# Optimization experiments

Measured on AMD Instinct MI355X. Metric: run time of the kernel, lower is better.

The kernel has to match this reference:

```python
import jax, jax.numpy as jnp
import numpy as np
from jax.scipy.special import logsumexp

N = 4096          # nodes per graph
E = 65536         # edges per graph
HID = 128
HEADS = 4
HD = HID // HEADS
L_GNN = 2
L_CROSS = 3
SINK_ITERS = 20
LN_EPS = 1e-5
SCALE = 1.0 / np.sqrt(HD)


def layer_norm(x, g, b):
    m = jnp.mean(x, axis=-1, keepdims=True)
    v = jnp.mean((x - m) ** 2, axis=-1, keepdims=True)
    return (x - m) * jax.lax.rsqrt(v + LN_EPS) * g + b


def gcn_conv(x, ei, w, b):
    # PyG GCNConv: self-loops + symmetric normalization, sum aggregation
    n = x.shape[0]
    xl = x @ w                                  # [n, hid]
    loops = jnp.arange(n, dtype=ei.dtype)
    src = jnp.concatenate([ei[0], loops])
    dst = jnp.concatenate([ei[1], loops])
    deg = jax.ops.segment_sum(jnp.ones_like(src, dtype=x.dtype), dst, num_segments=n)
    dinv = jnp.where(deg > 0, jax.lax.rsqrt(deg), 0.0)
    norm = dinv[src] * dinv[dst]                # [E+n]
    msg = xl[src] * norm[:, None]
    return jax.ops.segment_sum(msg, dst, num_segments=n) + b


def encode(x, ei, gcn_w, gcn_b, ln_g, ln_b):
    h = x
    for l in range(L_GNN):
        h = gcn_conv(h, ei, gcn_w[l], gcn_b[l])
        h = layer_norm(h, ln_g[l], ln_b[l])
        h = jax.nn.relu(h)
    return h


def attend(X, Y, wq, wk, wv, wo, bo):
    # X attends to Y; residual add
    n, m = X.shape[0], Y.shape[0]
    Q = (X @ wq).reshape(n, HEADS, HD).transpose(1, 0, 2)   # [h, n, d]
    K = (Y @ wk).reshape(m, HEADS, HD).transpose(1, 0, 2)
    V = (Y @ wv).reshape(m, HEADS, HD).transpose(1, 0, 2)
    scores = jnp.einsum('hnd,hmd->hnm', Q, K) * SCALE
    attn = jax.nn.softmax(scores, axis=-1)
    O = jnp.einsum('hnm,hmd->hnd', attn, V)                 # [h, n, d]
    O = O.transpose(1, 0, 2).reshape(n, HID)
    return O @ wo + bo + X


def sinkhorn(log_alpha, n_iters=SINK_ITERS):
    def body(i, lp):
        lp = lp - logsumexp(lp, axis=1, keepdims=True)  # row normalize
        lp = lp - logsumexp(lp, axis=0, keepdims=True)  # col normalize
        return lp
    log_p = jax.lax.fori_loop(0, n_iters, body, log_alpha)
    return jnp.exp(log_p)


def setup_inputs() -> dict:
    key = jax.random.key(0)
    ks = jax.random.split(key, 24)
    f32 = jnp.float32
    w = lambda k, *s: jax.random.normal(k, s, dtype=f32) * 0.05
    inp = {
        'A_x': jax.random.normal(ks[0], (N, HID), dtype=f32),
        'A_ei': jax.random.randint(ks[1], (2, E), 0, N),
        'B_x': jax.random.normal(ks[2], (N, HID), dtype=f32),
        'B_ei': jax.random.randint(ks[3], (2, E), 0, N),
        'in_proj_w': w(ks[4], HID, HID),
        'in_proj_b': jnp.zeros((HID,), f32),
        'gcn_w': w(ks[5], L_GNN, HID, HID),
        'gcn_b': jnp.zeros((L_GNN, HID), f32),
        'gcn_ln_g': jnp.ones((L_GNN, HID), f32),
        'gcn_ln_b': jnp.zeros((L_GNN, HID), f32),
        'cross_q': w(ks[6], L_CROSS, HID, HID),
        'cross_k': w(ks[7], L_CROSS, HID, HID),
        'cross_v': w(ks[8], L_CROSS, HID, HID),
        'cross_o': w(ks[9], L_CROSS, HID, HID),
        'cross_o_b': jnp.zeros((L_CROSS, HID), f32),
        'post_ln_g': jnp.ones((HID,), f32),
        'post_ln_b': jnp.zeros((HID,), f32),
        'proj_w': w(ks[10], HID, HID),
        'proj_b': jnp.zeros((HID,), f32),
        'null_vec': jax.random.normal(ks[11], (HID,), dtype=f32) * 0.01,
        'cp_w1': w(ks[12], HID, HID),
        'cp_b1': jnp.zeros((HID,), f32),
        'cp_w2': w(ks[13], HID, HID),
        'cp_b2': jnp.zeros((HID,), f32),
    }
    return inp


def reference(A_x, A_ei, B_x, B_ei, in_proj_w, in_proj_b, gcn_w, gcn_b,
              gcn_ln_g, gcn_ln_b, cross_q, cross_k, cross_v, cross_o,
              cross_o_b, post_ln_g, post_ln_b, proj_w, proj_b, null_vec,
              cp_w1, cp_b1, cp_w2, cp_b2):
    A_in = A_x @ in_proj_w + in_proj_b
    B_in = B_x @ in_proj_w + in_proj_b
    A_h = encode(A_in, A_ei, gcn_w, gcn_b, gcn_ln_g, gcn_ln_b)
    B_h = encode(B_in, B_ei, gcn_w, gcn_b, gcn_ln_g, gcn_ln_b)
    for l in range(L_CROSS):
        A_new = attend(A_h, B_h, cross_q[l], cross_k[l], cross_v[l], cross_o[l], cross_o_b[l])
        B_new = attend(B_h, A_h, cross_q[l], cross_k[l], cross_v[l], cross_o[l], cross_o_b[l])
        A_h, B_h = A_new, B_new
    A_h = layer_norm(A_h, post_ln_g, post_ln_b)
    B_h = layer_norm(B_h, post_ln_g, post_ln_b)
    A_p = A_h @ proj_w + proj_b
    B_p = B_h @ proj_w + proj_b
    inv_sqrt_d = 1.0 / np.sqrt(HID)
    logits = (A_p @ B_p.T) * inv_sqrt_d                    # [N, N]
    null_col = (A_p @ null_vec) * inv_sqrt_d               # [N]
    logits_with_null = jnp.concatenate([logits, null_col[:, None]], axis=1)
    P = sinkhorn(logits_with_null)
    zA = jax.nn.relu(A_p @ cp_w1 + cp_b1) @ cp_w2 + cp_b2
    zB = jax.nn.relu(B_p @ cp_w1 + cp_b1) @ cp_w2 + cp_b2
    return (logits_with_null, P, zA, zB)
```

## Files before the change

kernel.cpp:

```cpp
#include <hip/hip_runtime.h>
#include <hip/hip_bf16.h>
#include <math.h>

#define NN 4096
#define EE 65536
#define HID_ 128
#define HDIM 32
#define NCOL 4097
#define EHP 4104

static constexpr float SCALE_ATT = 0.17677669529663687f;
static constexpr float INV_SQRT_D = 0.08838834764831845f;
static constexpr float LOG2E = 1.4426950408889634f;

typedef __attribute__((ext_vector_type(8))) short bf16x8;
typedef __attribute__((ext_vector_type(4))) float f32x4;
typedef _Float16 half8 __attribute__((ext_vector_type(8)));
typedef _Float16 half4v __attribute__((ext_vector_type(4)));

__device__ __forceinline__ float wred64(float v) {
#pragma unroll
  for (int m = 32; m > 0; m >>= 1) v += __shfl_xor(v, m, 64);
  return v;
}

__device__ __forceinline__ ushort f2b(float f) {
  __hip_bfloat16 h = __float2bfloat16(f);
  union { __hip_bfloat16 h; ushort u; } c;
  c.h = h;
  return c.u;
}

__device__ __forceinline__ unsigned pack2bf(float e0, float e1) {
  return ((__float_as_uint(e1) + 0x8000u) & 0xffff0000u) |
         ((__float_as_uint(e0) + 0x8000u) >> 16);
}

template <bool BIAS, bool RELU, bool RESID, bool BCAST>
__global__ __launch_bounds__(256, 2) void gemm128_k(
    const float* __restrict__ x0, const float* __restrict__ x1,
    const float* __restrict__ w, const float* __restrict__ bias,
    const float* __restrict__ res0, const float* __restrict__ res1,
    float* __restrict__ o0, float* __restrict__ o1,
    ushort* __restrict__ ob0, ushort* __restrict__ ob1) {
  const float* x = blockIdx.y ? x1 : x0;
  const float* res = blockIdx.y ? res1 : res0;
  float* out = blockIdx.y ? o1 : o0;
  ushort* outb = blockIdx.y ? ob1 : ob0;
  __shared__ float Xs[32][132];
  __shared__ float Ws[32][128];
  const int tid = threadIdx.x;
  const int rowbase = blockIdx.x * 32;
#pragma unroll
  for (int i = 0; i < 4; ++i) {
    int lin = tid + i * 256;
    int r = lin >> 5, c4 = lin & 31;
    *(float4*)&Xs[r][c4 * 4] =
        *(const float4*)&x[(size_t)(rowbase + r) * HID_ + c4 * 4];
  }
  float acc[4][4] = {};
  const int tr = tid >> 5, tc = tid & 31;
  const int r0 = tr * 4, c0 = tc * 4;
  for (int k0 = 0; k0 < 128; k0 += 32) {
    __syncthreads();
#pragma unroll
    for (int i = 0; i < 4; ++i) {
      int lin = tid + i * 256;
      int r = lin >> 5, c4 = lin & 31;
      *(float4*)&Ws[r][c4 * 4] =
          *(const float4*)&w[(size_t)(k0 + r) * HID_ + c4 * 4];
    }
    __syncthreads();
#pragma unroll
    for (int kk = 0; kk < 32; kk += 4) {
      float4 wv0 = *(const float4*)&Ws[kk + 0][c0];
      float4 wv1 = *(const float4*)&Ws[kk + 1][c0];
      float4 wv2 = *(const float4*)&Ws[kk + 2][c0];
      float4 wv3 = *(const float4*)&Ws[kk + 3][c0];
#pragma unroll
      for (int r = 0; r < 4; ++r) {
        float4 xv = *(const float4*)&Xs[r0 + r][k0 + kk];
        acc[r][0] += xv.x * wv0.x + xv.y * wv1.x + xv.z * wv2.x + xv.w * wv3.x;
        acc[r][1] += xv.x * wv0.y + xv.y * wv1.y + xv.z * wv2.y + xv.w * wv3.y;
        acc[r][2] += xv.x * wv0.z + xv.y * wv1.z + xv.z * wv2.z + xv.w * wv3.z;
        acc[r][3] += xv.x * wv0.w + xv.y * wv1.w + xv.z * wv2.w + xv.w * wv3.w;
      }
    }
  }
  float4 bv = make_float4(0.f, 0.f, 0.f, 0.f);
  if (BIAS) bv = *(const float4*)&bias[c0];
#pragma unroll
  for (int r = 0; r < 4; ++r) {
    size_t orow = (size_t)(rowbase + r0 + r) * HID_ + c0;
    float4 ov;
    ov.x = acc[r][0] + bv.x;
    ov.y = acc[r][1] + bv.y;
    ov.z = acc[r][2] + bv.z;
    ov.w = acc[r][3] + bv.w;
    if (RESID) {
      float4 rv = *(const float4*)&res[orow];
      ov.x += rv.x; ov.y += rv.y; ov.z += rv.z; ov.w += rv.w;
    }
    if (RELU) {
      ov.x = fmaxf(ov.x, 0.f); ov.y = fmaxf(ov.y, 0.f);
      ov.z = fmaxf(ov.z, 0.f); ov.w = fmaxf(ov.w, 0.f);
    }
    *(float4*)&out[orow] = ov;
    if (BCAST) {
      *(ushort4*)&outb[orow] =
          make_ushort4(f2b(ov.x), f2b(ov.y), f2b(ov.z), f2b(ov.w));
    }
  }
}

__global__ __launch_bounds__(256, 2) void gemm_qkv_k(
    const float* __restrict__ x0, const float* __restrict__ x1,
    const float* __restrict__ wq, const float* __restrict__ wk,
    const float* __restrict__ wv, ushort* __restrict__ QA,
    ushort* __restrict__ QB, ushort* __restrict__ KA, ushort* __restrict__ KB,
    ushort* __restrict__ VA, ushort* __restrict__ VB) {
  const int z = blockIdx.z;
  const float* x = blockIdx.y ? x1 : x0;
  const float* w = (z == 0) ? wq : (z == 1 ? wk : wv);
  ushort* out = (z == 0) ? (blockIdx.y ? QB : QA)
                         : (z == 1 ? (blockIdx.y ? KB : KA)
                                   : (blockIdx.y ? VB : VA));
  const float scale = (z == 0) ? SCALE_ATT * LOG2E : 1.f;
  __shared__ float Xs[32][132];
  __shared__ float Ws[32][128];
  const int tid = threadIdx.x;
  const int rowbase = blockIdx.x * 32;
#pragma unroll
  for (int i = 0; i < 4; ++i) {
    int lin = tid + i * 256;
    int r = lin >> 5, c4 = lin & 31;
    *(float4*)&Xs[r][c4 * 4] =
        *(const float4*)&x[(size_t)(rowbase + r) * HID_ + c4 * 4];
  }
  float acc[4][4] = {};
  const int tr = tid >> 5, tc = tid & 31;
  const int r0 = tr * 4, c0 = tc * 4;
  for (int k0 = 0; k0 < 128; k0 += 32) {
    __syncthreads();
#pragma unroll
    for (int i = 0; i < 4; ++i) {
      int lin = tid + i * 256;
      int r = lin >> 5, c4 = lin & 31;
      *(float4*)&Ws[r][c4 * 4] =
          *(const float4*)&w[(size_t)(k0 + r) * HID_ + c4 * 4];
    }
    __syncthreads();
#pragma unroll
    for (int kk = 0; kk < 32; kk += 4) {
      float4 wv0 = *(const float4*)&Ws[kk + 0][c0];
      float4 wv1 = *(const float4*)&Ws[kk + 1][c0];
      float4 wv2 = *(const float4*)&Ws[kk + 2][c0];
      float4 wv3 = *(const float4*)&Ws[kk + 3][c0];
#pragma unroll
      for (int r = 0; r < 4; ++r) {
        float4 xv = *(const float4*)&Xs[r0 + r][k0 + kk];
        acc[r][0] += xv.x * wv0.x + xv.y * wv1.x + xv.z * wv2.x + xv.w * wv3.x;
        acc[r][1] += xv.x * wv0.y + xv.y * wv1.y + xv.z * wv2.y + xv.w * wv3.y;
        acc[r][2] += xv.x * wv0.z + xv.y * wv1.z + xv.z * wv2.z + xv.w * wv3.z;
        acc[r][3] += xv.x * wv0.w + xv.y * wv1.w + xv.z * wv2.w + xv.w * wv3.w;
      }
    }
  }
  if (z < 2) {
#pragma unroll
    for (int r = 0; r < 4; ++r) {
      ushort4 pk = make_ushort4(
          f2b(acc[r][0] * scale), f2b(acc[r][1] * scale),
          f2b(acc[r][2] * scale), f2b(acc[r][3] * scale));
      *(ushort4*)&out[(size_t)(rowbase + r0 + r) * HID_ + c0] = pk;
    }
  } else {
#pragma unroll
    for (int r = 0; r < 4; ++r)
#pragma unroll
      for (int c = 0; c < 4; ++c)
        out[(size_t)(c0 + c) * NN + rowbase + r0 + r] = f2b(acc[r][c]);
  }
}

__global__ void count_deg_k(const int* __restrict__ eiA,
                            const int* __restrict__ eiB, int* cntA, int* cntB) {
  int e = blockIdx.x * 256 + threadIdx.x;
  const int* ei = blockIdx.y ? eiB : eiA;
  int* cnt = blockIdx.y ? cntB : cntA;
  atomicAdd(&cnt[ei[EE + e]], 1);
}

__global__ __launch_bounds__(1024) void scan_k(const int* cntA, const int* cntB,
                                               int* rpA, int* rpB, float* dinvA,
                                               float* dinvB) {
  const int* cnt = blockIdx.y ? cntB : cntA;
  int* rp = blockIdx.y ? rpB : rpA;
  float* dinv = blockIdx.y ? dinvB : dinvA;
  __shared__ int part[1024];
  int tid = threadIdx.x;
  int v0 = cnt[tid * 4], v1 = cnt[tid * 4 + 1], v2 = cnt[tid * 4 + 2],
      v3 = cnt[tid * 4 + 3];
  int tot = v0 + v1 + v2 + v3;
  part[tid] = tot;
  __syncthreads();
  int x = tot;
  for (int off = 1; off < 1024; off <<= 1) {
    int y = (tid >= off) ? part[tid - off] : 0;
    __syncthreads();
    x += y;
    part[tid] = x;
    __syncthreads();
  }
  int excl = x - tot;
  rp[tid * 4] = excl;
  rp[tid * 4 + 1] = excl + v0;
  rp[tid * 4 + 2] = excl + v0 + v1;
  rp[tid * 4 + 3] = excl + v0 + v1 + v2;
  if (tid == 1023) rp[4096] = x;
  dinv[tid * 4] = rsqrtf((float)(v0 + 1));
  dinv[tid * 4 + 1] = rsqrtf((float)(v1 + 1));
  dinv[tid * 4 + 2] = rsqrtf((float)(v2 + 1));
  dinv[tid * 4 + 3] = rsqrtf((float)(v3 + 1));
}

__global__ void fill_k(const int* __restrict__ eiA, const int* __restrict__ eiB,
                       const int* rpA, const int* rpB, int* fillA, int* fillB,
                       int* srcA, int* srcB) {
  int e = blockIdx.x * 256 + threadIdx.x;
  const int* ei = blockIdx.y ? eiB : eiA;
  const int* rp = blockIdx.y ? rpB : rpA;
  int* fill = blockIdx.y ? fillB : fillA;
  int* src = blockIdx.y ? srcB : srcA;
  int d = ei[EE + e], s = ei[e];
  int pos = atomicAdd(&fill[d], 1);
  src[rp[d] + pos] = s;
}

__global__ __launch_bounds__(256) void gcn_agg_k(
    const float* __restrict__ xlA, const float* __restrict__ xlB,
    const int* __restrict__ rpA, const int* __restrict__ rpB,
    const int* __restrict__ srcA, const int* __restrict__ srcB,
    const float* __restrict__ dinvA, const float* __restrict__ dinvB,
    const float* __restrict__ gb, const float* __restrict__ lg,
    const float* __restrict__ lb, float* __restrict__ outA,
    float* __restrict__ outB) {
  const float* xl = blockIdx.y ? xlB : xlA;
  const int* rp = blockIdx.y ? rpB : rpA;
  const int* src = blockIdx.y ? srcB : srcA;
  const float* dinv = blockIdx.y ? dinvB : dinvA;
  float* out = blockIdx.y ? outB : outA;
  int wid = threadIdx.x >> 6, lane = threadIdx.x & 63;
  int node = blockIdx.x * 4 + wid;
  int b = rp[node], e = rp[node + 1];
  float di = dinv[node];
  float a0 = 0.f, a1 = 0.f;
  for (int base = b; base < e; base += 64) {
    int rem = e - base;
    int sv = 0;
    float wv = 0.f;
    if (lane < rem) {
      int s = src[base + lane];
      sv = s;
      wv = dinv[s] * di;
    }
    int nch = rem < 64 ? rem : 64;
    for (int j = 0; j < nch; ++j) {
      int s = __shfl(sv, j, 64);
      float w = __shfl(wv, j, 64);
      a0 += xl[(size_t)s * HID_ + lane] * w;
      a1 += xl[(size_t)s * HID_ + 64 + lane] * w;
    }
  }
  a0 += xl[(size_t)node * HID_ + lane] * di * di;
  a1 += xl[(size_t)node * HID_ + 64 + lane] * di * di;
  a0 += gb[lane];
  a1 += gb[64 + lane];
  float mean = wred64(a0 + a1) * (1.f / 128.f);
  float d0 = a0 - mean, d1 = a1 - mean;
  float var = wred64(d0 * d0 + d1 * d1) * (1.f / 128.f);
  float rs = rsqrtf(var + 1e-5f);
  float o0 = d0 * rs * lg[lane] + lb[lane];
  float o1 = d1 * rs * lg[64 + lane] + lb[64 + lane];
  out[(size_t)node * HID_ + lane] = fmaxf(o0, 0.f);
  out[(size_t)node * HID_ + 64 + lane] = fmaxf(o1, 0.f);
}

__global__ __launch_bounds__(256) void ln_k(float* __restrict__ hA,
                                            float* __restrict__ hB,
                                            const float* __restrict__ g,
                                            const float* __restrict__ b) {
  float* h = blockIdx.y ? hB : hA;
  int wid = threadIdx.x >> 6, lane = threadIdx.x & 63;
  int row = blockIdx.x * 4 + wid;
  float a0 = h[(size_t)row * HID_ + lane];
  float a1 = h[(size_t)row * HID_ + 64 + lane];
  float mean = wred64(a0 + a1) * (1.f / 128.f);
  float d0 = a0 - mean, d1 = a1 - mean;
  float var = wred64(d0 * d0 + d1 * d1) * (1.f / 128.f);
  float rs = rsqrtf(var + 1e-5f);
  h[(size_t)row * HID_ + lane] = d0 * rs * g[lane] + b[lane];
  h[(size_t)row * HID_ + 64 + lane] = d1 * rs * g[64 + lane] + b[64 + lane];
}

__global__ __launch_bounds__(256, 4) void attn_mfma_k(
    const ushort* __restrict__ QA, const ushort* __restrict__ KA,
    const ushort* __restrict__ VtA, const ushort* __restrict__ QB,
    const ushort* __restrict__ KB, const ushort* __restrict__ VtB,
    float* __restrict__ Opart, float* __restrict__ lpart) {
  const int qt = blockIdx.x, h = blockIdx.y;
  const int dir = blockIdx.z >> 1, sl = blockIdx.z & 1;
  const ushort* Q = dir ? QB : QA;
  const ushort* K = dir ? KA : KB;
  const ushort* Vt = dir ? VtA : VtB;

  __shared__ ushort KF[2048];
  __shared__ ushort VF[2048];
  __shared__ ushort PF[4][1024];

  const int tid = threadIdx.x;
  const int w = tid >> 6, l = tid & 63;
  const int lr = l & 15, lg = l >> 4;

  const int qrow = qt * 64 + w * 16 + lr;
  bf16x8 qf = *(const bf16x8*)&Q[(size_t)qrow * HID_ + h * HDIM + lg * 8];

  f32x4 oacc0 = {0.f, 0.f, 0.f, 0.f};
  f32x4 oacc1 = {0.f, 0.f, 0.f, 0.f};
  float lsum = 0.f;

  const int ldst = ((w * 4 + lg) * 16 + lr) * 8;
  const ushort* Kg =
      K + (size_t)(sl * 2048 + w * 16 + lr) * HID_ + h * HDIM + lg * 8;
  const ushort* Vg = Vt + (size_t)(h * HDIM + (w >> 1) * 16 + lr) * NN +
                     sl * 2048 + (w & 1) * 32 + lg * 8;

  bf16x8 kreg = *(const bf16x8*)Kg;
  bf16x8 vreg = *(const bf16x8*)Vg;

  for (int t = 0; t < 32; ++t) {
    __syncthreads();
    *(bf16x8*)&KF[ldst] = kreg;
    *(bf16x8*)&VF[ldst] = vreg;
    if (t < 31) {
      kreg = *(const bf16x8*)&Kg[(size_t)(t + 1) * 64 * HID_];
      vreg = *(const bf16x8*)&Vg[(t + 1) * 64];
    }
    __syncthreads();
#pragma unroll
    for (int s = 0; s < 4; ++s) {
      bf16x8 kf = *(const bf16x8*)&KF[((s * 4 + lg) * 16 + lr) * 8];
      f32x4 c = {0.f, 0.f, 0.f, 0.f};
      c = __builtin_amdgcn_mfma_f32_16x16x32_bf16(kf, qf, c, 0, 0, 0);
      float e0 = exp2f(c[0]), e1 = exp2f(c[1]);
      float e2 = exp2f(c[2]), e3 = exp2f(c[3]);
      lsum += (e0 + e1) + (e2 + e3);
      const int k0 = s >> 1;
      const int lgr = (s & 1) * 2 + (lg >> 1);
      const int e8 = (lg & 1) * 4;
      *(uint2*)&PF[w][((k0 * 4 + lgr) * 16 + lr) * 8 + e8] =
          make_uint2(pack2bf(e0, e1), pack2bf(e2, e3));
    }
#pragma unroll
    for (int k0 = 0; k0 < 2; ++k0) {
      bf16x8 pa = *(const bf16x8*)&PF[w][((k0 * 4 + lg) * 16 + lr) * 8];
      bf16x8 vb0 = *(const bf16x8*)&VF[((k0 * 4 + lg) * 16 + lr) * 8];
      bf16x8 vb1 = *(const bf16x8*)&VF[(((2 + k0) * 4 + lg) * 16 + lr) * 8];
      oacc0 = __builtin_amdgcn_mfma_f32_16x16x32_bf16(pa, vb0, oacc0, 0, 0, 0);
      oacc1 = __builtin_amdgcn_mfma_f32_16x16x32_bf16(pa, vb1, oacc1, 0, 0, 0);
    }
  }
  lsum += __shfl_xor(lsum, 16, 64);
  lsum += __shfl_xor(lsum, 32, 64);
  const int pb = sl * 2 + dir;
  if (lg == 0)
    lpart[(size_t)(pb * 4 + h) * NN + qt * 64 + w * 16 + lr] = lsum;
#pragma unroll
  for (int r = 0; r < 4; ++r) {
    int q = qt * 64 + w * 16 + lg * 4 + r;
    Opart[((size_t)pb * NN + q) * HID_ + h * HDIM + lr] = oacc0[r];
    Opart[((size_t)pb * NN + q) * HID_ + h * HDIM + 16 + lr] = oacc1[r];
  }
}

__global__ void attn_combine_k(const float* __restrict__ Opart,
                               const float* __restrict__ lpart,
                               float* __restrict__ outA,
                               float* __restrict__ outB) {
  int row = blockIdx.x, dir = blockIdx.y, f = threadIdx.x;
  int h = f >> 5;
  float o = 0.f, lsum = 0.f;
#pragma unroll
  for (int sl = 0; sl < 2; ++sl) {
    int pb = sl * 2 + dir;
    o += Opart[((size_t)pb * NN + row) * HID_ + f];
    lsum += lpart[(size_t)(pb * 4 + h) * NN + row];
  }
  float* out = dir ? outB : outA;
  out[(size_t)row * HID_ + f] = o / lsum;
}

__global__ __launch_bounds__(256, 2) void gemm_nt_mfma_k(
    const ushort* __restrict__ Apb, const ushort* __restrict__ Bpb,
    float* __restrict__ L, _Float16* __restrict__ Eh) {
  __shared__ ushort As[128 * 128];
  __shared__ ushort Bs[128 * 128];
  const int tid = threadIdx.x;
  const int ab = blockIdx.y * 128, bb = blockIdx.x * 128;
#pragma unroll
  for (int i = 0; i < 8; ++i) {
    int lin = tid + i * 256;
    int row = lin >> 4, ch = lin & 15;
    int pch = ch ^ (row & 15);
    *(bf16x8*)&As[row * 128 + pch * 8] =
        *(const bf16x8*)&Apb[(size_t)(ab + row) * HID_ + ch * 8];
    *(bf16x8*)&Bs[row * 128 + pch * 8] =
        *(const bf16x8*)&Bpb[(size_t)(bb + row) * HID_ + ch * 8];
  }
  __syncthreads();
  const int w = tid >> 6, l = tid & 63, lr = l & 15, lg = l >> 4;
  f32x4 acc[2][8];
#pragma unroll
  for (int fm = 0; fm < 2; ++fm)
#pragma unroll
    for (int nf = 0; nf < 8; ++nf) acc[fm][nf] = {0.f, 0.f, 0.f, 0.f};
#pragma unroll
  for (int kc = 0; kc < 4; ++kc) {
    bf16x8 a0 = *(const bf16x8*)
        &As[((w * 2 + 0) * 16 + lr) * 128 + ((kc * 4 + lg) ^ lr) * 8];
    bf16x8 a1 = *(const bf16x8*)
        &As[((w * 2 + 1) * 16 + lr) * 128 + ((kc * 4 + lg) ^ lr) * 8];
#pragma unroll
    for (int nf = 0; nf < 8; ++nf) {
      bf16x8 bf = *(const bf16x8*)
          &Bs[(nf * 16 + lr) * 128 + ((kc * 4 + lg) ^ lr) * 8];
      acc[0][nf] = __builtin_amdgcn_mfma_f32_16x16x32_bf16(a0, bf, acc[0][nf], 0, 0, 0);
      acc[1][nf] = __builtin_amdgcn_mfma_f32_16x16x32_bf16(a1, bf, acc[1][nf], 0, 0, 0);
    }
  }
#pragma unroll
  for (int fm = 0; fm < 2; ++fm)
#pragma unroll
    for (int nf = 0; nf < 8; ++nf)
#pragma unroll
      for (int r = 0; r < 4; ++r) {
        int row = ab + (w * 2 + fm) * 16 + lg * 4 + r;
        int col = bb + nf * 16 + lr;
        float v = acc[fm][nf][r] * INV_SQRT_D;
        L[(size_t)row * NCOL + col] = v;
        Eh[(size_t)row * EHP + col] = (_Float16)exp2f(v * LOG2E);
      }
}

__global__ void null_col_k(const float* __restrict__ Ap,
                           const float* __restrict__ nv, float* __restrict__ L,
                           _Float16* __restrict__ Eh) {
  int row = blockIdx.x, lane = threadIdx.x;
  float s = Ap[(size_t)row * HID_ + lane] * nv[lane] +
            Ap[(size_t)row * HID_ + 64 + lane] * nv[64 + lane];
  s = wred64(s);
  if (lane == 0) {
    float v = s * INV_SQRT_D;
    L[(size_t)row * NCOL + 4096] = v;
    Eh[(size_t)row * EHP + 4096] = (_Float16)exp2f(v * LOG2E);
  }
  if (lane >= 1 && lane < 8) Eh[(size_t)row * EHP + 4096 + lane] = (_Float16)0.f;
}

__global__ __launch_bounds__(256) void sink_fused_k(
    const _Float16* __restrict__ Eh, const float* __restrict__ t_old,
    float* __restrict__ t_new, float* __restrict__ colpart,
    float* __restrict__ u) {
  __shared__ float vinv[EHP];
  __shared__ float uls[8];
  const int tid = threadIdx.x, bid = blockIdx.x;
  if (tid < 9) {
    int z = bid * 9 + tid;
    if (z < EHP) t_new[z] = 0.f;
  }
  for (int i = tid; i < EHP; i += 256)
    vinv[i] = (i < NCOL) ? (1.f / t_old[i]) : 0.f;
  __syncthreads();
  const int w = tid >> 6, l = tid & 63;
  const int row0 = bid * 8;
#pragma unroll
  for (int rr = 0; rr < 2; ++rr) {
    int row = row0 + w * 2 + rr;
    const _Float16* Ep = Eh + (size_t)row * EHP;
    float s = 0.f;
    for (int j = l * 4; j < EHP; j += 256) {
      half4v e = *(const half4v*)&Ep[j];
      float4 vv = *(const float4*)&vinv[j];
      s += (float)e[0] * vv.x + (float)e[1] * vv.y + (float)e[2] * vv.z +
           (float)e[3] * vv.w;
    }
    s = wred64(s);
    if (l == 0) {
      float uv = 1.f / s;
      uls[w * 2 + rr] = uv;
      u[row] = uv;
    }
  }
  __syncthreads();
  float ur[8];
#pragma unroll
  for (int r = 0; r < 8; ++r) ur[r] = uls[r];
  float* cp = colpart + (size_t)bid * EHP;
  for (int j = tid * 4; j < EHP; j += 1024) {
    float a0 = 0.f, a1 = 0.f, a2 = 0.f, a3 = 0.f;
#pragma unroll
    for (int r = 0; r < 8; ++r) {
      half4v e = *(const half4v*)&Eh[(size_t)(row0 + r) * EHP + j];
      a0 += (float)e[0] * ur[r];
      a1 += (float)e[1] * ur[r];
      a2 += (float)e[2] * ur[r];
      a3 += (float)e[3] * ur[r];
    }
    *(float4*)&cp[j] = make_float4(a0, a1, a2, a3);
  }
}

__global__ __launch_bounds__(256) void sink_reduce_k(
    const float* __restrict__ colpart, float* __restrict__ t_new) {
  int j = blockIdx.x * 256 + threadIdx.x;
  if (j >= EHP) return;
  int b0 = blockIdx.y * 64;
  float s = 0.f;
#pragma unroll 8
  for (int b = 0; b < 64; ++b) s += colpart[(size_t)(b0 + b) * EHP + j];
  atomicAdd(&t_new[j], s);
}

__global__ void sink_init_k(float* t0) {
  int j = blockIdx.x * 256 + threadIdx.x;
  if (j < EHP) t0[j] = 1.f;
}

__global__ __launch_bounds__(256) void sink_finalE_k(
    const _Float16* __restrict__ Eh, const float* __restrict__ u,
    const float* __restrict__ t, float* __restrict__ P) {
  __shared__ float vls[NCOL];
  int tid = threadIdx.x, row = blockIdx.x;
  for (int i = tid; i < NCOL; i += 256) vls[i] = 1.f / t[i];
  __syncthreads();
  float ur = u[row];
  const _Float16* Ep = Eh + (size_t)row * EHP;
  float* Pp = P + (size_t)row * NCOL;
  for (int j = tid; j < NCOL; j += 256) Pp[j] = (float)Ep[j] * ur * vls[j];
}

extern "C" void kernel_launch(void* const* d_in, const int* in_sizes, int n_in,
                              void* d_out, int out_size, void* d_ws,
                              size_t ws_size, hipStream_t stream) {
  const float* A_x = (const float*)d_in[0];
  const int* A_ei = (const int*)d_in[1];
  const float* B_x = (const float*)d_in[2];
  const int* B_ei = (const int*)d_in[3];
  const float* in_w = (const float*)d_in[4];
  const float* in_b = (const float*)d_in[5];
  const float* gcn_w = (const float*)d_in[6];
  const float* gcn_b = (const float*)d_in[7];
  const float* lng = (const float*)d_in[8];
  const float* lnb = (const float*)d_in[9];
  const float* cq = (const float*)d_in[10];
  const float* ck = (const float*)d_in[11];
  const float* cv = (const float*)d_in[12];
  const float* co = (const float*)d_in[13];
  const float* cob = (const float*)d_in[14];
  const float* plg = (const float*)d_in[15];
  const float* plb = (const float*)d_in[16];
  const float* pw = (const float*)d_in[17];
  const float* pb = (const float*)d_in[18];
  const float* nullv = (const float*)d_in[19];
  const float* w1 = (const float*)d_in[20];
  const float* b1 = (const float*)d_in[21];
  const float* w2 = (const float*)d_in[22];
  const float* b2 = (const float*)d_in[23];

  float* ws = (float*)d_ws;
  size_t off = 0;
  auto alloc = [&](size_t n) { float* p = ws + off; off += n; return p; };
  const size_t NHE = (size_t)NN * HID_;
  float* tA = alloc(NHE);
  float* tB = alloc(NHE);
  float* Ap = alloc(NHE);
  float* Bp = alloc(NHE);
  ushort* Apb = (ushort*)alloc(NHE / 2);
  ushort* Bpb = (ushort*)alloc(NHE / 2);
  float* uvec = alloc(NN);
  float* t0 = alloc(EHP);
  float* t1 = alloc(EHP);
  float* zone = ws + off;
  float* hA0 = alloc(NHE); float* hB0 = alloc(NHE);
  float* hA1 = alloc(NHE); float* hB1 = alloc(NHE);
  float* QA = alloc(NHE);  float* KAb = alloc(NHE); float* VAb = alloc(NHE);
  float* QB = alloc(NHE);  float* KBb = alloc(NHE); float* VBb = alloc(NHE);
  float* Opart = alloc(4 * NHE);
  float* lpart = alloc((size_t)16 * NN);
  float* dinvA = alloc(NN); float* dinvB = alloc(NN);
  int* ib = (int*)(ws + off);
  int* cntA = ib;             int* cntB = cntA + NN;
  int* fillA = cntB + NN;     int* fillB = fillA + NN;
  int* rpA = fillB + NN;      int* rpB = rpA + (NN + 1);
  int* srcA = rpB + (NN + 1); int* srcB = srcA + EE;
  size_t ints_floats = (size_t)(4 * NN + 2 * (NN + 1) + 2 * EE);
  _Float16* Eh = (_Float16*)zone;
  {
    size_t named = (size_t)((ws + off) - zone) + ints_floats;
    size_t eh_floats = ((size_t)NN * EHP + 1) / 2;
    size_t need = eh_floats > named ? eh_floats : named;
    off = (size_t)(zone - ws) + need;
  }
  float* colpart = alloc((size_t)512 * EHP);

  float* Lout = (float*)d_out;
  float* Pout = Lout + (size_t)NN * NCOL;
  float* zA = Pout + (size_t)NN * NCOL;
  float* zB = zA + NHE;

  hipMemsetAsync(cntA, 0, 4 * NN * sizeof(int), stream);

  gemm128_k<true, false, false, false><<<dim3(128, 2), 256, 0, stream>>>(
      A_x, B_x, in_w, in_b, nullptr, nullptr, hA0, hB0, nullptr, nullptr);
  count_deg_k<<<dim3(256, 2), 256, 0, stream>>>(A_ei, B_ei, cntA, cntB);
  scan_k<<<dim3(1, 2), 1024, 0, stream>>>(cntA, cntB, rpA, rpB, dinvA, dinvB);
  fill_k<<<dim3(256, 2), 256, 0, stream>>>(A_ei, B_ei, rpA, rpB, fillA, fillB,
                                           srcA, srcB);
  float* hA = hA0; float* hB = hB0; float* aA = hA1; float* aB = hB1;
  for (int l = 0; l < 2; ++l) {
    gemm128_k<false, false, false, false><<<dim3(128, 2), 256, 0, stream>>>(
        hA, hB, gcn_w + (size_t)l * HID_ * HID_, nullptr, nullptr, nullptr, tA,
        tB, nullptr, nullptr);
    gcn_agg_k<<<dim3(1024, 2), 256, 0, stream>>>(
        tA, tB, rpA, rpB, srcA, srcB, dinvA, dinvB, gcn_b + l * HID_,
        lng + l * HID_, lnb + l * HID_, hA, hB);
  }
  for (int l = 0; l < 3; ++l) {
    const float* wq = cq + (size_t)l * HID_ * HID_;
    const float* wk = ck + (size_t)l * HID_ * HID_;
    const float* wv = cv + (size_t)l * HID_ * HID_;
    const float* wo = co + (size_t)l * HID_ * HID_;
    gemm_qkv_k<<<dim3(128, 2, 3), 256, 0, stream>>>(
        hA, hB, wq, wk, wv, (ushort*)QA, (ushort*)QB, (ushort*)KAb,
        (ushort*)KBb, (ushort*)VAb, (ushort*)VBb);
    attn_mfma_k<<<dim3(64, 4, 4), 256, 0, stream>>>(
        (ushort*)QA, (ushort*)KAb, (ushort*)VAb, (ushort*)QB, (ushort*)KBb,
        (ushort*)VBb, Opart, lpart);
    attn_combine_k<<<dim3(NN, 2), 128, 0, stream>>>(Opart, lpart, tA, tB);
    gemm128_k<true, false, true, false><<<dim3(128, 2), 256, 0, stream>>>(
        tA, tB, wo, cob + l * HID_, hA, hB, aA, aB, nullptr, nullptr);
    float* t;
    t = hA; hA = aA; aA = t;
    t = hB; hB = aB; aB = t;
  }
  ln_k<<<dim3(1024, 2), 256, 0, stream>>>(hA, hB, plg, plb);
  gemm128_k<true, false, false, true><<<dim3(128, 2), 256, 0, stream>>>(
      hA, hB, pw, pb, nullptr, nullptr, Ap, Bp, Apb, Bpb);
  gemm_nt_mfma_k<<<dim3(32, 32), 256, 0, stream>>>(Apb, Bpb, Lout, Eh);
  null_col_k<<<NN, 64, 0, stream>>>(Ap, nullv, Lout, Eh);
  sink_init_k<<<17, 256, 0, stream>>>(t0);
  float* tb[2] = {t0, t1};
  for (int it = 0; it < 20; ++it) {
    float* told = tb[it & 1];
    float* tnew = tb[(it + 1) & 1];
    sink_fused_k<<<512, 256, 0, stream>>>(Eh, told, tnew, colpart, uvec);
    sink_reduce_k<<<dim3(17, 8), 256, 0, stream>>>(colpart, tnew);
  }
  sink_finalE_k<<<NN, 256, 0, stream>>>(Eh, uvec, tb[0], Pout);
  gemm128_k<true, true, false, false><<<dim3(128, 2), 256, 0, stream>>>(
      Ap, Bp, w1, b1, nullptr, nullptr, tA, tB, nullptr, nullptr);
  gemm128_k<true, false, false, false><<<dim3(128, 2), 256, 0, stream>>>(
      tA, tB, w2, b2, nullptr, nullptr, zA, zB, nullptr, nullptr);
}
```

Measured before the change: 1.017 ms.

## Move 128-wide GEMMs to split-bf16 MFMA, fuse attention combine, retile Sinkhorn

All 128x128 dense GEMMs now run on MFMA using a three-term hi/lo bf16 split to keep near-fp32 accuracy. Weights are transposed and split once per call by a new prep kernel. The attention partial-combine kernel is folded into the output-projection GEMM's input load, removing one launch and one round trip through memory. Separately, the Sinkhorn fused kernel processes 16 rows per block instead of 8, which halves the column-partial buffer and the reduce work but also halves the number of blocks.

New measurement: 1.079 ms. 6.1% more time.

```diff
diff --git a/kernel.cpp b/kernel.cpp
--- a/kernel.cpp
+++ b/kernel.cpp
@@ -36,150 +36,241 @@
          ((__float_as_uint(e0) + 0x8000u) >> 16);
 }
 
-template <bool BIAS, bool RELU, bool RESID, bool BCAST>
-__global__ __launch_bounds__(256, 2) void gemm128_k(
+__global__ void wprep_k(const float* __restrict__ in_w,
+                        const float* __restrict__ gcn_w,
+                        const float* __restrict__ cq,
+                        const float* __restrict__ ck,
+                        const float* __restrict__ cv,
+                        const float* __restrict__ co,
+                        const float* __restrict__ pw,
+                        const float* __restrict__ w1,
+                        const float* __restrict__ w2, ushort* __restrict__ wth,
+                        ushort* __restrict__ wtl) {
+  int s = blockIdx.y;
+  const float* W = s == 0    ? in_w
+                   : s < 3   ? gcn_w + (size_t)(s - 1) * 16384
+                   : s < 6   ? cq + (size_t)(s - 3) * 16384
+                   : s < 9   ? ck + (size_t)(s - 6) * 16384
+                   : s < 12  ? cv + (size_t)(s - 9) * 16384
+                   : s < 15  ? co + (size_t)(s - 12) * 16384
+                   : s == 15 ? pw
+                   : s == 16 ? w1
+                             : w2;
+  int n0 = blockIdx.x * 16;
+  int tid = threadIdx.x;
+#pragma unroll
+  for (int i = 0; i < 8; ++i) {
+    int idx = tid + i * 256;
+    int k = idx & 127, nn = idx >> 7;
+    float v = W[(size_t)k * 128 + n0 + nn];
+    ushort h = f2b(v);
+    float hf = __uint_as_float((unsigned)h << 16);
+    ushort lo = f2b(v - hf);
+    size_t o = (size_t)s * 16384 + (size_t)(n0 + nn) * 128 + k;
+    wth[o] = h;
+    wtl[o] = lo;
+  }
+}
+
+template <bool BIAS, bool RELU, bool RESID, bool BF16OUT, bool COMBINE>
+__global__ __launch_bounds__(256) void gemm_mfma_k(
     const float* __restrict__ x0, const float* __restrict__ x1,
-    const float* __restrict__ w, const float* __restrict__ bias,
+    const float* __restrict__ lp, const ushort* __restrict__ wth,
+    const ushort* __restrict__ wtl, const float* __restrict__ bias,
     const float* __restrict__ res0, const float* __restrict__ res1,
-    float* __restrict__ o0, float* __restrict__ o1,
-    ushort* __restrict__ ob0, ushort* __restrict__ ob1) {
-  const float* x = blockIdx.y ? x1 : x0;
-  const float* res = blockIdx.y ? res1 : res0;
-  float* out = blockIdx.y ? o1 : o0;
-  ushort* outb = blockIdx.y ? ob1 : ob0;
-  __shared__ float Xs[32][132];
-  __shared__ float Ws[32][128];
+    float* __restrict__ o0, float* __restrict__ o1, ushort* __restrict__ ob0,
+    ushort* __restrict__ ob1) {
+  __shared__ ushort Xh[32 * 128], Xl[32 * 128];
+  __shared__ ushort Whs[64 * 128], Wls[64 * 128];
   const int tid = threadIdx.x;
-  const int rowbase = blockIdx.x * 32;
-#pragma unroll
-  for (int i = 0; i < 4; ++i) {
-    int lin = tid + i * 256;
-    int r = lin >> 5, c4 = lin & 31;
-    *(float4*)&Xs[r][c4 * 4] =
-        *(const float4*)&x[(size_t)(rowbase + r) * HID_ + c4 * 4];
-  }
-  float acc[4][4] = {};
-  const int tr = tid >> 5, tc = tid & 31;
-  const int r0 = tr * 4, c0 = tc * 4;
-  for (int k0 = 0; k0 < 128; k0 += 32) {
+  const int dir = blockIdx.y;
+  const int m0 = blockIdx.x * 32;
+  const float* res = dir ? res1 : res0;
+  float* out = dir ? o1 : o0;
+  ushort* outb = dir ? ob1 : ob0;
+
+  {
+    const float* x = dir ? x1 : x0;
+#pragma unroll
+    for (int i = 0; i < 2; ++i) {
+      int c = tid + i * 256;
+      int row = c >> 4, ch = c & 15;
+      int rowg = m0 + row;
+      float v[8];
+      if (COMBINE) {
+        int hh = ch >> 2;
+        float ls = lp[((size_t)(dir * 4 + hh)) * NN + rowg] +
+                   lp[((size_t)((2 + dir) * 4 + hh)) * NN + rowg];
+        float inv = 1.f / ls;
+        const float* p0 = &x0[((size_t)dir * NN + rowg) * HID_ + ch * 8];
+        const float* p1 = &x0[((size_t)(2 + dir) * NN + rowg) * HID_ + ch * 8];
+        float4 a0 = *(const float4*)p0, a1 = *(const float4*)(p0 + 4);
+        float4 b0 = *(const float4*)p1, b1 = *(const float4*)(p1 + 4);
+        v[0] = (a0.x + b0.x) * inv; v[1] = (a0.y + b0.y) * inv;
+        v[2] = (a0.z + b0.z) * inv; v[3] = (a0.w + b0.w) * inv;
+        v[4] = (a1.x + b1.x) * inv; v[5] = (a1.y + b1.y) * inv;
+        v[6] = (a1.z + b1.z) * inv; v[7] = (a1.w + b1.w) * inv;
+      } else {
+        float4 a0 = *(const float4*)&x[(size_t)rowg * HID_ + ch * 8];
+        float4 a1 = *(const float4*)&x[(size_t)rowg * HID_ + ch * 8 + 4];
+        v[0] = a0.x; v[1] = a0.y; v[2] = a0.z; v[3] = a0.w;
+        v[4] = a1.x; v[5] = a1.y; v[6] = a1.z; v[7] = a1.w;
+      }
+      union { ushort u[8]; bf16x8 vv; } H, L;
+#pragma unroll
+      for (int e = 0; e < 8; ++e) {
+        ushort h = f2b(v[e]);
+        float hf = __uint_as_float((unsigned)h << 16);
+        H.u[e] = h;
+        L.u[e] = f2b(v[e] - hf);
+      }
+      int pch = ch ^ (row & 15);
+      *(bf16x8*)&Xh[row * 128 + pch * 8] = H.vv;
+      *(bf16x8*)&Xl[row * 128 + pch * 8] = L.vv;
+    }
+  }
+
+  const int w = tid >> 6, l = tid & 63, lr = l & 15, lg = l >> 4;
+  const int mrow = (w & 1) * 16 + lr;
+  const int nb = (w >> 1) * 2;
+
+#pragma unroll
+  for (int nh = 0; nh < 2; ++nh) {
+    if (nh) __syncthreads();
+#pragma unroll
+    for (int i = 0; i < 4; ++i) {
+      int c = tid + i * 256;
+      int row = c >> 4, ch = c & 15;
+      int pch = ch ^ (row & 15);
+      *(bf16x8*)&Whs[row * 128 + pch * 8] =
+          *(const bf16x8*)&wth[(size_t)(nh * 64 + row) * 128 + ch * 8];
+      *(bf16x8*)&Wls[row * 128 + pch * 8] =
+          *(const bf16x8*)&wtl[(size_t)(nh * 64 + row) * 128 + ch * 8];
+    }
     __syncthreads();
+    f32x4 acc0 = {0.f, 0.f, 0.f, 0.f}, acc1 = {0.f, 0.f, 0.f, 0.f};
+#pragma unroll
+    for (int kc = 0; kc < 4; ++kc) {
+      int chx = ((kc * 4 + lg) ^ lr) * 8;
+      bf16x8 ah = *(const bf16x8*)&Xh[mrow * 128 + chx];
+      bf16x8 al = *(const bf16x8*)&Xl[mrow * 128 + chx];
+      bf16x8 bh0 = *(const bf16x8*)&Whs[(nb * 16 + lr) * 128 + chx];
+      bf16x8 bl0 = *(const bf16x8*)&Wls[(nb * 16 + lr) * 128 + chx];
+      bf16x8 bh1 = *(const bf16x8*)&Whs[((nb + 1) * 16 + lr) * 128 + chx];
+      bf16x8 bl1 = *(const bf16x8*)&Wls[((nb + 1) * 16 + lr) * 128 + chx];
+      acc0 = __builtin_amdgcn_mfma_f32_16x16x32_bf16(ah, bh0, acc0, 0, 0, 0);
+      acc0 = __builtin_amdgcn_mfma_f32_16x16x32_bf16(al, bh0, acc0, 0, 0, 0);
+      acc0 = __builtin_amdgcn_mfma_f32_16x16x32_bf16(ah, bl0, acc0, 0, 0, 0);
+      acc1 = __builtin_amdgcn_mfma_f32_16x16x32_bf16(ah, bh1, acc1, 0, 0, 0);
+      acc1 = __builtin_amdgcn_mfma_f32_16x16x32_bf16(al, bh1, acc1, 0, 0, 0);
+      acc1 = __builtin_amdgcn_mfma_f32_16x16x32_bf16(ah, bl1, acc1, 0, 0, 0);
+    }
+#pragma unroll
+    for (int j = 0; j < 2; ++j) {
+      const f32x4 a = j ? acc1 : acc0;
+      int col = nh * 64 + (nb + j) * 16 + lr;
+      float bv = BIAS ? bias[col] : 0.f;
+#pragma unroll
+      for (int r = 0; r < 4; ++r) {
+        int rowg = m0 + (w & 1) * 16 + lg * 4 + r;
+        float val = a[r] + bv;
+        if (RESID) val += res[(size_t)rowg * HID_ + col];
+        if (RELU) val = fmaxf(val, 0.f);
+        out[(size_t)rowg * HID_ + col] = val;
+        if (BF16OUT) outb[(size_t)rowg * HID_ + col] = f2b(val);
+      }
+    }
+  }
+}
+
+__global__ __launch_bounds__(256) void gemm_qkv_mfma_k(
+    const float* __restrict__ x0, const float* __restrict__ x1,
+    const ushort* __restrict__ wthQ, const ushort* __restrict__ wtlQ,
+    const ushort* __restrict__ wthK, const ushort* __restrict__ wtlK,
+    const ushort* __restrict__ wthV, const ushort* __restrict__ wtlV,
+    ushort* __restrict__ QA, ushort* __restrict__ QB, ushort* __restrict__ KA,
+    ushort* __restrict__ KB, ushort* __restrict__ VA,
+    ushort* __restrict__ VB) {
+  __shared__ ushort Xh[32 * 128], Xl[32 * 128];
+  __shared__ ushort Whs[64 * 128], Wls[64 * 128];
+  const int tid = threadIdx.x;
+  const int dir = blockIdx.y, z = blockIdx.z;
+  const int m0 = blockIdx.x * 32;
+  const ushort* wth = z == 0 ? wthQ : (z == 1 ? wthK : wthV);
+  const ushort* wtl = z == 0 ? wtlQ : (z == 1 ? wtlK : wtlV);
+  ushort* out = z == 0 ? (dir ? QB : QA)
+                       : (z == 1 ? (dir ? KB : KA) : (dir ? VB : VA));
+  const float scale = (z == 0) ? SCALE_ATT * LOG2E : 1.f;
+  {
+    const float* x = dir ? x1 : x0;
+#pragma unroll
+    for (int i = 0; i < 2; ++i) {
+      int c = tid + i * 256;
+      int row = c >> 4, ch = c & 15;
+      int rowg = m0 + row;
+      float4 a0 = *(const float4*)&x[(size_t)rowg * HID_ + ch * 8];
+      float4 a1 = *(const float4*)&x[(size_t)rowg * HID_ + ch * 8 + 4];
+      float v[8] = {a0.x, a0.y, a0.z, a0.w, a1.x, a1.y, a1.z, a1.w};
+      union { ushort u[8]; bf16x8 vv; } H, L;
+#pragma unroll
+      for (int e = 0; e < 8; ++e) {
+        ushort h = f2b(v[e]);
+        float hf = __uint_as_float((unsigned)h << 16);
+        H.u[e] = h;
+        L.u[e] = f2b(v[e] - hf);
+      }
+      int pch = ch ^ (row & 15);
+      *(bf16x8*)&Xh[row * 128 + pch * 8] = H.vv;
+      *(bf16x8*)&Xl[row * 128 + pch * 8] = L.vv;
+    }
+  }
+  const int w = tid >> 6, l = tid & 63, lr = l & 15, lg = l >> 4;
+  const int mrow = (w & 1) * 16 + lr;
+  const int nb = (w >> 1) * 2;
+#pragma unroll
+  for (int nh = 0; nh < 2; ++nh) {
+    if (nh) __syncthreads();
 #pragma unroll
     for (int i = 0; i < 4; ++i) {
-      int lin = tid + i * 256;
-      int r = lin >> 5, c4 = lin & 31;
-      *(float4*)&Ws[r][c4 * 4] =
-          *(const float4*)&w[(size_t)(k0 + r) * HID_ + c4 * 4];
+      int c = tid + i * 256;
+      int row = c >> 4, ch = c & 15;
+      int pch = ch ^ (row & 15);
+      *(bf16x8*)&Whs[row * 128 + pch * 8] =
+          *(const bf16x8*)&wth[(size_t)(nh * 64 + row) * 128 + ch * 8];
+      *(bf16x8*)&Wls[row * 128 + pch * 8] =
+          *(const bf16x8*)&wtl[(size_t)(nh * 64 + row) * 128 + ch * 8];
     }
     __syncthreads();
-#pragma unroll
-    for (int kk = 0; kk < 32; kk += 4) {
-      float4 wv0 = *(const float4*)&Ws[kk + 0][c0];
-      float4 wv1 = *(const float4*)&Ws[kk + 1][c0];
-      float4 wv2 = *(const float4*)&Ws[kk + 2][c0];
-      float4 wv3 = *(const float4*)&Ws[kk + 3][c0];
+    f32x4 acc0 = {0.f, 0.f, 0.f, 0.f}, acc1 = {0.f, 0.f, 0.f, 0.f};
+#pragma unroll
+    for (int kc = 0; kc < 4; ++kc) {
+      int chx = ((kc * 4 + lg) ^ lr) * 8;
+      bf16x8 ah = *(const bf16x8*)&Xh[mrow * 128 + chx];
+      bf16x8 al = *(const bf16x8*)&Xl[mrow * 128 + chx];
+      bf16x8 bh0 = *(const bf16x8*)&Whs[(nb * 16 + lr) * 128 + chx];
+      bf16x8 bl0 = *(const bf16x8*)&Wls[(nb * 16 + lr) * 128 + chx];
+      bf16x8 bh1 = *(const bf16x8*)&Whs[((nb + 1) * 16 + lr) * 128 + chx];
+      bf16x8 bl1 = *(const bf16x8*)&Wls[((nb + 1) * 16 + lr) * 128 + chx];
+      acc0 = __builtin_amdgcn_mfma_f32_16x16x32_bf16(ah, bh0, acc0, 0, 0, 0);
+      acc0 = __builtin_amdgcn_mfma_f32_16x16x32_bf16(al, bh0, acc0, 0, 0, 0);
+      acc0 = __builtin_amdgcn_mfma_f32_16x16x32_bf16(ah, bl0, acc0, 0, 0, 0);
+      acc1 = __builtin_amdgcn_mfma_f32_16x16x32_bf16(ah, bh1, acc1, 0, 0, 0);
+      acc1 = __builtin_amdgcn_mfma_f32_16x16x32_bf16(al, bh1, acc1, 0, 0, 0);
+      acc1 = __builtin_amdgcn_mfma_f32_16x16x32_bf16(ah, bl1, acc1, 0, 0, 0);
+    }
+#pragma unroll
+    for (int j = 0; j < 2; ++j) {
+      const f32x4 a = j ? acc1 : acc0;
+      int col = nh * 64 + (nb + j) * 16 + lr;
 #pragma unroll
       for (int r = 0; r < 4; ++r) {
-        float4 xv = *(const float4*)&Xs[r0 + r][k0 + kk];
-        acc[r][0] += xv.x * wv0.x + xv.y * wv1.x + xv.z * wv2.x + xv.w * wv3.x;
-        acc[r][1] += xv.x * wv0.y + xv.y * wv1.y + xv.z * wv2.y + xv.w * wv3.y;
-        acc[r][2] += xv.x * wv0.z + xv.y * wv1.z + xv.z * wv2.z + xv.w * wv3.z;
-        acc[r][3] += xv.x * wv0.w + xv.y * wv1.w + xv.z * wv2.w + xv.w * wv3.w;
+        int rowg = m0 + (w & 1) * 16 + lg * 4 + r;
+        if (z < 2)
+          out[(size_t)rowg * HID_ + col] = f2b(a[r] * scale);
+        else
+          out[(size_t)col * NN + rowg] = f2b(a[r]);
       }
     }
-  }
-  float4 bv = make_float4(0.f, 0.f, 0.f, 0.f);
-  if (BIAS) bv = *(const float4*)&bias[c0];
-#pragma unroll
-  for (int r = 0; r < 4; ++r) {
-    size_t orow = (size_t)(rowbase + r0 + r) * HID_ + c0;
-    float4 ov;
-    ov.x = acc[r][0] + bv.x;
-    ov.y = acc[r][1] + bv.y;
-    ov.z = acc[r][2] + bv.z;
-    ov.w = acc[r][3] + bv.w;
-    if (RESID) {
-      float4 rv = *(const float4*)&res[orow];
-      ov.x += rv.x; ov.y += rv.y; ov.z += rv.z; ov.w += rv.w;
-    }
-    if (RELU) {
-      ov.x = fmaxf(ov.x, 0.f); ov.y = fmaxf(ov.y, 0.f);
-      ov.z = fmaxf(ov.z, 0.f); ov.w = fmaxf(ov.w, 0.f);
-    }
-    *(float4*)&out[orow] = ov;
-    if (BCAST) {
-      *(ushort4*)&outb[orow] =
-          make_ushort4(f2b(ov.x), f2b(ov.y), f2b(ov.z), f2b(ov.w));
-    }
-  }
-}
-
-__global__ __launch_bounds__(256, 2) void gemm_qkv_k(
-    const float* __restrict__ x0, const float* __restrict__ x1,
-    const float* __restrict__ wq, const float* __restrict__ wk,
-    const float* __restrict__ wv, ushort* __restrict__ QA,
-    ushort* __restrict__ QB, ushort* __restrict__ KA, ushort* __restrict__ KB,
-    ushort* __restrict__ VA, ushort* __restrict__ VB) {
-  const int z = blockIdx.z;
-  const float* x = blockIdx.y ? x1 : x0;
-  const float* w = (z == 0) ? wq : (z == 1 ? wk : wv);
-  ushort* out = (z == 0) ? (blockIdx.y ? QB : QA)
-                         : (z == 1 ? (blockIdx.y ? KB : KA)
-                                   : (blockIdx.y ? VB : VA));
-  const float scale = (z == 0) ? SCALE_ATT * LOG2E : 1.f;
-  __shared__ float Xs[32][132];
-  __shared__ float Ws[32][128];
-  const int tid = threadIdx.x;
-  const int rowbase = blockIdx.x * 32;
-#pragma unroll
-  for (int i = 0; i < 4; ++i) {
-    int lin = tid + i * 256;
-    int r = lin >> 5, c4 = lin & 31;
-    *(float4*)&Xs[r][c4 * 4] =
-        *(const float4*)&x[(size_t)(rowbase + r) * HID_ + c4 * 4];
-  }
-  float acc[4][4] = {};
-  const int tr = tid >> 5, tc = tid & 31;
-  const int r0 = tr * 4, c0 = tc * 4;
-  for (int k0 = 0; k0 < 128; k0 += 32) {
-    __syncthreads();
-#pragma unroll
-    for (int i = 0; i < 4; ++i) {
-      int lin = tid + i * 256;
-      int r = lin >> 5, c4 = lin & 31;
-      *(float4*)&Ws[r][c4 * 4] =
-          *(const float4*)&w[(size_t)(k0 + r) * HID_ + c4 * 4];
-    }
-    __syncthreads();
-#pragma unroll
-    for (int kk = 0; kk < 32; kk += 4) {
-      float4 wv0 = *(const float4*)&Ws[kk + 0][c0];
-      float4 wv1 = *(const float4*)&Ws[kk + 1][c0];
-      float4 wv2 = *(const float4*)&Ws[kk + 2][c0];
-      float4 wv3 = *(const float4*)&Ws[kk + 3][c0];
-#pragma unroll
-      for (int r = 0; r < 4; ++r) {
-        float4 xv = *(const float4*)&Xs[r0 + r][k0 + kk];
-        acc[r][0] += xv.x * wv0.x + xv.y * wv1.x + xv.z * wv2.x + xv.w * wv3.x;
-        acc[r][1] += xv.x * wv0.y + xv.y * wv1.y + xv.z * wv2.y + xv.w * wv3.y;
-        acc[r][2] += xv.x * wv0.z + xv.y * wv1.z + xv.z * wv2.z + xv.w * wv3.z;
-        acc[r][3] += xv.x * wv0.w + xv.y * wv1.w + xv.z * wv2.w + xv.w * wv3.w;
-      }
-    }
-  }
-  if (z < 2) {
-#pragma unroll
-    for (int r = 0; r < 4; ++r) {
-      ushort4 pk = make_ushort4(
-          f2b(acc[r][0] * scale), f2b(acc[r][1] * scale),
-          f2b(acc[r][2] * scale), f2b(acc[r][3] * scale));
-      *(ushort4*)&out[(size_t)(rowbase + r0 + r) * HID_ + c0] = pk;
-    }
-  } else {
-#pragma unroll
-    for (int r = 0; r < 4; ++r)
-#pragma unroll
-      for (int c = 0; c < 4; ++c)
-        out[(size_t)(c0 + c) * NN + rowbase + r0 + r] = f2b(acc[r][c]);
   }
 }
 
@@ -383,23 +474,6 @@
   }
 }
 
-__global__ void attn_combine_k(const float* __restrict__ Opart,
-                               const float* __restrict__ lpart,
-                               float* __restrict__ outA,
-                               float* __restrict__ outB) {
-  int row = blockIdx.x, dir = blockIdx.y, f = threadIdx.x;
-  int h = f >> 5;
-  float o = 0.f, lsum = 0.f;
-#pragma unroll
-  for (int sl = 0; sl < 2; ++sl) {
-    int pb = sl * 2 + dir;
-    o += Opart[((size_t)pb * NN + row) * HID_ + f];
-    lsum += lpart[(size_t)(pb * 4 + h) * NN + row];
-  }
-  float* out = dir ? outB : outA;
-  out[(size_t)row * HID_ + f] = o / lsum;
-}
-
 __global__ __launch_bounds__(256, 2) void gemm_nt_mfma_k(
     const ushort* __restrict__ Apb, const ushort* __restrict__ Bpb,
     float* __restrict__ L, _Float16* __restrict__ Eh) {
@@ -472,20 +546,20 @@
     float* __restrict__ t_new, float* __restrict__ colpart,
     float* __restrict__ u) {
   __shared__ float vinv[EHP];
-  __shared__ float uls[8];
+  __shared__ float uls[16];
   const int tid = threadIdx.x, bid = blockIdx.x;
-  if (tid < 9) {
-    int z = bid * 9 + tid;
+  if (bid < 17) {
+    int z = bid * 256 + tid;
     if (z < EHP) t_new[z] = 0.f;
   }
   for (int i = tid; i < EHP; i += 256)
     vinv[i] = (i < NCOL) ? (1.f / t_old[i]) : 0.f;
   __syncthreads();
   const int w = tid >> 6, l = tid & 63;
-  const int row0 = bid * 8;
-#pragma unroll
-  for (int rr = 0; rr < 2; ++rr) {
-    int row = row0 + w * 2 + rr;
+  const int row0 = bid * 16;
+#pragma unroll
+  for (int rr = 0; rr < 4; ++rr) {
+    int row = row0 + w * 4 + rr;
     const _Float16* Ep = Eh + (size_t)row * EHP;
     float s = 0.f;
     for (int j = l * 4; j < EHP; j += 256) {
@@ -497,19 +571,19 @@
     s = wred64(s);
     if (l == 0) {
       float uv = 1.f / s;
-      uls[w * 2 + rr] = uv;
+      uls[w * 4 + rr] = uv;
       u[row] = uv;
     }
   }
   __syncthreads();
-  float ur[8];
-#pragma unroll
-  for (int r = 0; r < 8; ++r) ur[r] = uls[r];
+  float ur[16];
+#pragma unroll
+  for (int r = 0; r < 16; ++r) ur[r] = uls[r];
   float* cp = colpart + (size_t)bid * EHP;
   for (int j = tid * 4; j < EHP; j += 1024) {
     float a0 = 0.f, a1 = 0.f, a2 = 0.f, a3 = 0.f;
 #pragma unroll
-    for (int r = 0; r < 8; ++r) {
+    for (int r = 0; r < 16; ++r) {
       half4v e = *(const half4v*)&Eh[(size_t)(row0 + r) * EHP + j];
       a0 += (float)e[0] * ur[r];
       a1 += (float)e[1] * ur[r];
@@ -524,10 +598,10 @@
     const float* __restrict__ colpart, float* __restrict__ t_new) {
   int j = blockIdx.x * 256 + threadIdx.x;
   if (j >= EHP) return;
-  int b0 = blockIdx.y * 64;
+  int b0 = blockIdx.y * 32;
   float s = 0.f;
 #pragma unroll 8
-  for (int b = 0; b < 64; ++b) s += colpart[(size_t)(b0 + b) * EHP + j];
+  for (int b = 0; b < 32; ++b) s += colpart[(size_t)(b0 + b) * EHP + j];
   atomicAdd(&t_new[j], s);
 }
 
@@ -587,6 +661,8 @@
   float* Bp = alloc(NHE);
   ushort* Apb = (ushort*)alloc(NHE / 2);
   ushort* Bpb = (ushort*)alloc(NHE / 2);
+  ushort* WThi = (ushort*)alloc((size_t)18 * 16384 / 2);
+  ushort* WTlo = (ushort*)alloc((size_t)18 * 16384 / 2);
   float* uvec = alloc(NN);
   float* t0 = alloc(EHP);
   float* t1 = alloc(EHP);
@@ -611,7 +687,7 @@
     size_t need = eh_floats > named ? eh_floats : named;
     off = (size_t)(zone - ws) + need;
   }
-  float* colpart = alloc((size_t)512 * EHP);
+  float* colpart = alloc((size_t)256 * EHP);
 
   float* Lout = (float*)d_out;
   float* Pout = Lout + (size_t)NN * NCOL;
@@ -620,42 +696,52 @@
 
   hipMemsetAsync(cntA, 0, 4 * NN * sizeof(int), stream);
 
-  gemm128_k<true, false, false, false><<<dim3(128, 2), 256, 0, stream>>>(
-      A_x, B_x, in_w, in_b, nullptr, nullptr, hA0, hB0, nullptr, nullptr);
+  wprep_k<<<dim3(8, 18), 256, 0, stream>>>(in_w, gcn_w, cq, ck, cv, co, pw, w1,
+                                           w2, WThi, WTlo);
+  gemm_mfma_k<true, false, false, false, false>
+      <<<dim3(128, 2), 256, 0, stream>>>(A_x, B_x, nullptr, WThi, WTlo, in_b,
+                                         nullptr, nullptr, hA0, hB0, nullptr,
+                                         nullptr);
   count_deg_k<<<dim3(256, 2), 256, 0, stream>>>(A_ei, B_ei, cntA, cntB);
   scan_k<<<dim3(1, 2), 1024, 0, stream>>>(cntA, cntB, rpA, rpB, dinvA, dinvB);
   fill_k<<<dim3(256, 2), 256, 0, stream>>>(A_ei, B_ei, rpA, rpB, fillA, fillB,
                                            srcA, srcB);
   float* hA = hA0; float* hB = hB0; float* aA = hA1; float* aB = hB1;
   for (int l = 0; l < 2; ++l) {
-    gemm128_k<false, false, false, false><<<dim3(128, 2), 256, 0, stream>>>(
-        hA, hB, gcn_w + (size_t)l * HID_ * HID_, nullptr, nullptr, nullptr, tA,
-        tB, nullptr, nullptr);
+    gemm_mfma_k<false, false, false, false, false>
+        <<<dim3(128, 2), 256, 0, stream>>>(
+            hA, hB, nullptr, WThi + (size_t)16384 * (1 + l),
+            WTlo + (size_t)16384 * (1 + l), nullptr, nullptr, nullptr, tA, tB,
+            nullptr, nullptr);
     gcn_agg_k<<<dim3(1024, 2), 256, 0, stream>>>(
         tA, tB, rpA, rpB, srcA, srcB, dinvA, dinvB, gcn_b + l * HID_,
         lng + l * HID_, lnb + l * HID_, hA, hB);
   }
   for (int l = 0; l < 3; ++l) {
-    const float* wq = cq + (size_t)l * HID_ * HID_;
-    const float* wk = ck + (size_t)l * HID_ * HID_;
-    const float* wv = cv + (size_t)l * HID_ * HID_;
-    const float* wo = co + (size_t)l * HID_ * HID_;
-    gemm_qkv_k<<<dim3(128, 2, 3), 256, 0, stream>>>(
-        hA, hB, wq, wk, wv, (ushort*)QA, (ushort*)QB, (ushort*)KAb,
-        (ushort*)KBb, (ushort*)VAb, (ushort*)VBb);
+    gemm_qkv_mfma_k<<<dim3(128, 2, 3), 256, 0, stream>>>(
+        hA, hB, WThi + (size_t)16384 * (3 + l), WTlo + (size_t)16384 * (3 + l),
+        WThi + (size_t)16384 * (6 + l), WTlo + (size_t)16384 * (6 + l),
+        WThi + (size_t)16384 * (9 + l), WTlo + (size_t)16384 * (9 + l),
+        (ushort*)QA, (ushort*)QB, (ushort*)KAb, (ushort*)KBb, (ushort*)VAb,
+        (ushort*)VBb);
     attn_mfma_k<<<dim3(64, 4, 4), 256, 0, stream>>>(
         (ushort*)QA, (ushort*)KAb, (ushort*)VAb, (ushort*)QB, (ushort*)KBb,
         (ushort*)VBb, Opart, lpart);
-    attn_combine_k<<<dim3(NN, 2), 128, 0, stream>>>(Opart, lpart, tA, tB);
-    gemm128_k<true, false, true, false><<<dim3(128, 2), 256, 0, stream>>>(
-        tA, tB, wo, cob + l * HID_, hA, hB, aA, aB, nullptr, nullptr);
+    gemm_mfma_k<true, false, true, false, true>
+        <<<dim3(128, 2), 256, 0, stream>>>(
+            Opart, nullptr, lpart, WThi + (size_t)16384 * (12 + l),
+            WTlo + (size_t)16384 * (12 + l), cob + l * HID_, hA, hB, aA, aB,
+            nullptr, nullptr);
     float* t;
     t = hA; hA = aA; aA = t;
     t = hB; hB = aB; aB = t;
   }
   ln_k<<<dim3(1024, 2), 256, 0, stream>>>(hA, hB, plg, plb);
-  gemm128_k<true, false, false, true><<<dim3(128, 2), 256, 0, stream>>>(
-      hA, hB, pw, pb, nullptr, nullptr, Ap, Bp, Apb, Bpb);
+  gemm_mfma_k<true, false, false, true, false>
+      <<<dim3(128, 2), 256, 0, stream>>>(hA, hB, nullptr,
+                                         WThi + (size_t)16384 * 15,
+                                         WTlo + (size_t)16384 * 15, pb, nullptr,
+                                         nullptr, Ap, Bp, Apb, Bpb);
   gemm_nt_mfma_k<<<dim3(32, 32), 256, 0, stream>>>(Apb, Bpb, Lout, Eh);
   null_col_k<<<NN, 64, 0, stream>>>(Ap, nullv, Lout, Eh);
   sink_init_k<<<17, 256, 0, stream>>>(t0);
@@ -663,12 +749,18 @@
   for (int it = 0; it < 20; ++it) {
     float* told = tb[it & 1];
     float* tnew = tb[(it + 1) & 1];
-    sink_fused_k<<<512, 256, 0, stream>>>(Eh, told, tnew, colpart, uvec);
+    sink_fused_k<<<256, 256, 0, stream>>>(Eh, told, tnew, colpart, uvec);
     sink_reduce_k<<<dim3(17, 8), 256, 0, stream>>>(colpart, tnew);
   }
   sink_finalE_k<<<NN, 256, 0, stream>>>(Eh, uvec, tb[0], Pout);
-  gemm128_k<true, true, false, false><<<dim3(128, 2), 256, 0, stream>>>(
-      Ap, Bp, w1, b1, nullptr, nullptr, tA, tB, nullptr, nullptr);
-  gemm128_k<true, false, false, false><<<dim3(128, 2), 256, 0, stream>>>(
-      tA, tB, w2, b2, nullptr, nullptr, zA, zB, nullptr, nullptr);
-}
+  gemm_mfma_k<true, true, false, false, false>
+      <<<dim3(128, 2), 256, 0, stream>>>(Ap, Bp, nullptr,
+                                         WThi + (size_t)16384 * 16,
+                                         WTlo + (size_t)16384 * 16, b1, nullptr,
+                                         nullptr, tA, tB, nullptr, nullptr);
+  gemm_mfma_k<true, false, false, false, false>
+      <<<dim3(128, 2), 256, 0, stream>>>(tA, tB, nullptr,
+                                         WThi + (size_t)16384 * 17,
+                                         WTlo + (size_t)16384 * 17, b2, nullptr,
+                                         nullptr, zA, zB, nullptr, nullptr);
+}
```
